# Kernel tuning notes

Hardware: AMD Instinct MI355X
Metric: run time of the kernel (lower is better)

Reference implementation:

```python
import jax, jax.numpy as jnp
import numpy as np

N = 100000
D = 512
B = 64
L = 2048

def setup_inputs() -> dict:
    key = jax.random.key(0)
    k1, k2, k3 = jax.random.split(key, 3)
    gcn_hidden = jax.random.normal(k1, (N, D), dtype=jnp.float32)
    token_position = jax.random.randint(k2, (2 * N,), 0, B, dtype=jnp.int64)
    token_position2 = jax.random.randint(k3, (2 * N,), 0, B, dtype=jnp.int64)
    return {
        "gcn_hidden": gcn_hidden,
        "token_position": token_position,
        "batch_size": B,
        "max_length": L,
        "token_position2": token_position2,
    }

def reference(gcn_hidden, token_position, batch_size, max_length, token_position2):
    # repeat each node row twice consecutively: [N, D] -> [2N, D]
    g2 = jnp.repeat(gcn_hidden, 2, axis=0)
    # scatter-sum rows into batch_size segments: [2N, D] -> [B, D]
    x = jax.ops.segment_sum(g2, token_position, num_segments=batch_size)
    # broadcast across sequence length: [B, D] -> [B, L, D]
    return jnp.broadcast_to(x[:, None, :], (batch_size, max_length, g2.shape[1]))
```

## Files before the change

### kernel.cpp

```cpp
#include <hip/hip_runtime.h>

#define D_DIM    512
#define B_DIM    64
#define L_DIM    2048
#define NBLK1    256
#define THREADS1 512
#define MAXCHUNK 512
#define XSZ      (B_DIM * D_DIM)

typedef float f32x4 __attribute__((ext_vector_type(4)));

__device__ __forceinline__ void rmw2(float* acc, int ia, int ib, float v) {
    float ra = acc[ia];
    float rb = acc[ib];
    float addb = (ia == ib) ? (v + v) : v;
    acc[ia] = ra + v;
    acc[ib] = rb + addb;
}

__global__ __launch_bounds__(THREADS1)
void seg_sum_kernel(const float* __restrict__ g, const int* __restrict__ tp,
                    float* __restrict__ dst, int N, int chunk, int use_atomic) {
    __shared__ float acc[XSZ];
    __shared__ int   pos[2 * MAXCHUNK];
    const int tid = threadIdx.x;

    for (int i = tid; i < XSZ; i += THREADS1) acc[i] = 0.0f;

    int start = blockIdx.x * chunk;
    int end   = start + chunk; if (end > N) end = N;
    int n     = end - start;
    for (int i = tid; i < 2 * n; i += THREADS1) pos[i] = tp[2 * start + i];
    __syncthreads();

    const float* gp = g + (size_t)start * D_DIM + tid;

    int i = 0;
    for (; i + 8 <= n; i += 8) {
        float v0 = gp[(size_t)(i + 0) * D_DIM];
        float v1 = gp[(size_t)(i + 1) * D_DIM];
        float v2 = gp[(size_t)(i + 2) * D_DIM];
        float v3 = gp[(size_t)(i + 3) * D_DIM];
        float v4 = gp[(size_t)(i + 4) * D_DIM];
        float v5 = gp[(size_t)(i + 5) * D_DIM];
        float v6 = gp[(size_t)(i + 6) * D_DIM];
        float v7 = gp[(size_t)(i + 7) * D_DIM];
        rmw2(acc, pos[2*i+ 0] * D_DIM + tid, pos[2*i+ 1] * D_DIM + tid, v0);
        rmw2(acc, pos[2*i+ 2] * D_DIM + tid, pos[2*i+ 3] * D_DIM + tid, v1);
        rmw2(acc, pos[2*i+ 4] * D_DIM + tid, pos[2*i+ 5] * D_DIM + tid, v2);
        rmw2(acc, pos[2*i+ 6] * D_DIM + tid, pos[2*i+ 7] * D_DIM + tid, v3);
        rmw2(acc, pos[2*i+ 8] * D_DIM + tid, pos[2*i+ 9] * D_DIM + tid, v4);
        rmw2(acc, pos[2*i+10] * D_DIM + tid, pos[2*i+11] * D_DIM + tid, v5);
        rmw2(acc, pos[2*i+12] * D_DIM + tid, pos[2*i+13] * D_DIM + tid, v6);
        rmw2(acc, pos[2*i+14] * D_DIM + tid, pos[2*i+15] * D_DIM + tid, v7);
    }
    for (; i < n; ++i) {
        float v = gp[(size_t)i * D_DIM];
        rmw2(acc, pos[2*i + 0] * D_DIM + tid, pos[2*i + 1] * D_DIM + tid, v);
    }
    __syncthreads();

    if (use_atomic) {
        for (int j = tid; j < XSZ; j += THREADS1) {
            float v = acc[j];
            if (v != 0.0f) atomicAdd(&dst[j], v);
        }
    } else {
        f32x4* outp = (f32x4*)(dst + (size_t)blockIdx.x * XSZ);
        const f32x4* a4 = (const f32x4*)acc;
        for (int j = tid; j < XSZ / 4; j += THREADS1) outp[j] = a4[j];
    }
}

__global__ __launch_bounds__(128)
void reduce_partials(const float* __restrict__ p, float* __restrict__ x) {
    int j = blockIdx.x * 128 + threadIdx.x;
    const float* pj = p + j;
    float s = 0.0f;
    #pragma unroll 8
    for (int k = 0; k < NBLK1; ++k) s += pj[(size_t)k * XSZ];
    x[j] = s;
}

#define BC_BLOCKS  1024
#define BC_THREADS 256
__global__ __launch_bounds__(BC_THREADS)
void bcast_lin(const float* __restrict__ x, f32x4* __restrict__ out) {
    int gw   = (blockIdx.x * BC_THREADS + threadIdx.x) >> 6;
    int lane = threadIdx.x & 63;
    size_t base = (size_t)gw * 4096;
    int b = (int)(base >> 18);

    const f32x4* x4 = (const f32x4*)x;
    f32x4 v0 = x4[(b << 7) | lane];
    f32x4 v1 = x4[(b << 7) | (64 + lane)];

    f32x4* o = out + base + lane;
    #pragma unroll 8
    for (int t = 0; t < 64; t += 2) {
        __builtin_nontemporal_store(v0, &o[(size_t)t * 64]);
        __builtin_nontemporal_store(v1, &o[(size_t)t * 64 + 64]);
    }
}

extern "C" void kernel_launch(void* const* d_in, const int* in_sizes, int n_in,
                              void* d_out, int out_size, void* d_ws, size_t ws_size,
                              hipStream_t stream) {
    const float* g   = (const float*)d_in[0];
    const int*   tp  = (const int*)d_in[1];
    float*       out = (float*)d_out;

    int N = in_sizes[1] / 2;
    int chunk = (N + NBLK1 - 1) / NBLK1;

    const size_t need = (size_t)(NBLK1 + 1) * XSZ * sizeof(float);

    if (ws_size >= need) {
        float* partials = (float*)d_ws;
        float* x        = partials + (size_t)NBLK1 * XSZ;
        seg_sum_kernel<<<NBLK1, THREADS1, 0, stream>>>(g, tp, partials, N, chunk, 0);
        reduce_partials<<<XSZ / 128, 128, 0, stream>>>(partials, x);
        bcast_lin<<<BC_BLOCKS, BC_THREADS, 0, stream>>>(x, (f32x4*)out);
    } else {
        float* x = (float*)d_ws;
        (void)hipMemsetAsync(d_ws, 0, XSZ * sizeof(float), stream);
        seg_sum_kernel<<<NBLK1, THREADS1, 0, stream>>>(g, tp, x, N, chunk, 1);
        bcast_lin<<<BC_BLOCKS, BC_THREADS, 0, stream>>>(x, (f32x4*)out);
    }
}
```

Baseline: 434.7 us.

## Split partial reduction across K groups and fold final sum into broadcast

The partial-sum reduction is split into KSPLIT=8 slices, giving 8x more blocks of 256 threads, each summing 32 partials instead of 256. The final 8-way sum moves into the broadcast kernel, which now loops over the parts before writing. Position pairs are loaded as int2 vectors from shared memory, and the broadcast stores change from nontemporal to ordinary stores. The aim is more parallelism in the short reduction kernel. The cost is extra reads in the broadcast kernel and possibly different cache behaviour on the large 33 MB output write.

```diff
diff --git a/kernel.cpp b/kernel.cpp
--- a/kernel.cpp
+++ b/kernel.cpp
@@ -7,6 +7,7 @@
 #define THREADS1 512
 #define MAXCHUNK 512
 #define XSZ      (B_DIM * D_DIM)
+#define KSPLIT   8
 
 typedef float f32x4 __attribute__((ext_vector_type(4)));
 
@@ -22,7 +23,7 @@
 void seg_sum_kernel(const float* __restrict__ g, const int* __restrict__ tp,
                     float* __restrict__ dst, int N, int chunk, int use_atomic) {
     __shared__ float acc[XSZ];
-    __shared__ int   pos[2 * MAXCHUNK];
+    __shared__ int2  pos2[MAXCHUNK];
     const int tid = threadIdx.x;
 
     for (int i = tid; i < XSZ; i += THREADS1) acc[i] = 0.0f;
@@ -30,7 +31,8 @@
     int start = blockIdx.x * chunk;
     int end   = start + chunk; if (end > N) end = N;
     int n     = end - start;
-    for (int i = tid; i < 2 * n; i += THREADS1) pos[i] = tp[2 * start + i];
+    const int2* tp2 = (const int2*)(tp + 2 * start);
+    for (int i = tid; i < n; i += THREADS1) pos2[i] = tp2[i];
     __syncthreads();
 
     const float* gp = g + (size_t)start * D_DIM + tid;
@@ -45,18 +47,21 @@
         float v5 = gp[(size_t)(i + 5) * D_DIM];
         float v6 = gp[(size_t)(i + 6) * D_DIM];
         float v7 = gp[(size_t)(i + 7) * D_DIM];
-        rmw2(acc, pos[2*i+ 0] * D_DIM + tid, pos[2*i+ 1] * D_DIM + tid, v0);
-        rmw2(acc, pos[2*i+ 2] * D_DIM + tid, pos[2*i+ 3] * D_DIM + tid, v1);
-        rmw2(acc, pos[2*i+ 4] * D_DIM + tid, pos[2*i+ 5] * D_DIM + tid, v2);
-        rmw2(acc, pos[2*i+ 6] * D_DIM + tid, pos[2*i+ 7] * D_DIM + tid, v3);
-        rmw2(acc, pos[2*i+ 8] * D_DIM + tid, pos[2*i+ 9] * D_DIM + tid, v4);
-        rmw2(acc, pos[2*i+10] * D_DIM + tid, pos[2*i+11] * D_DIM + tid, v5);
-        rmw2(acc, pos[2*i+12] * D_DIM + tid, pos[2*i+13] * D_DIM + tid, v6);
-        rmw2(acc, pos[2*i+14] * D_DIM + tid, pos[2*i+15] * D_DIM + tid, v7);
+        int2 p0 = pos2[i+0], p1 = pos2[i+1], p2 = pos2[i+2], p3 = pos2[i+3];
+        int2 p4 = pos2[i+4], p5 = pos2[i+5], p6 = pos2[i+6], p7 = pos2[i+7];
+        rmw2(acc, p0.x * D_DIM + tid, p0.y * D_DIM + tid, v0);
+        rmw2(acc, p1.x * D_DIM + tid, p1.y * D_DIM + tid, v1);
+        rmw2(acc, p2.x * D_DIM + tid, p2.y * D_DIM + tid, v2);
+        rmw2(acc, p3.x * D_DIM + tid, p3.y * D_DIM + tid, v3);
+        rmw2(acc, p4.x * D_DIM + tid, p4.y * D_DIM + tid, v4);
+        rmw2(acc, p5.x * D_DIM + tid, p5.y * D_DIM + tid, v5);
+        rmw2(acc, p6.x * D_DIM + tid, p6.y * D_DIM + tid, v6);
+        rmw2(acc, p7.x * D_DIM + tid, p7.y * D_DIM + tid, v7);
     }
     for (; i < n; ++i) {
         float v = gp[(size_t)i * D_DIM];
-        rmw2(acc, pos[2*i + 0] * D_DIM + tid, pos[2*i + 1] * D_DIM + tid, v);
+        int2 p = pos2[i];
+        rmw2(acc, p.x * D_DIM + tid, p.y * D_DIM + tid, v);
     }
     __syncthreads();
 
@@ -72,34 +77,40 @@
     }
 }
 
-__global__ __launch_bounds__(128)
-void reduce_partials(const float* __restrict__ p, float* __restrict__ x) {
-    int j = blockIdx.x * 128 + threadIdx.x;
-    const float* pj = p + j;
+__global__ __launch_bounds__(256)
+void reduce_partials(const float* __restrict__ p, float* __restrict__ xp) {
+    const int jblks = XSZ / 256;
+    int jblk = blockIdx.x & (jblks - 1);
+    int ks   = blockIdx.x >> 7;
+    int j    = (jblk << 8) + threadIdx.x;
+    const float* pj = p + j + (size_t)ks * (NBLK1 / KSPLIT) * XSZ;
     float s = 0.0f;
     #pragma unroll 8
-    for (int k = 0; k < NBLK1; ++k) s += pj[(size_t)k * XSZ];
-    x[j] = s;
+    for (int k = 0; k < NBLK1 / KSPLIT; ++k) s += pj[(size_t)k * XSZ];
+    xp[(size_t)ks * XSZ + j] = s;
 }
 
 #define BC_BLOCKS  1024
 #define BC_THREADS 256
 __global__ __launch_bounds__(BC_THREADS)
-void bcast_lin(const float* __restrict__ x, f32x4* __restrict__ out) {
+void bcast_lin(const float* __restrict__ xp, int nparts, f32x4* __restrict__ out) {
     int gw   = (blockIdx.x * BC_THREADS + threadIdx.x) >> 6;
     int lane = threadIdx.x & 63;
     size_t base = (size_t)gw * 4096;
     int b = (int)(base >> 18);
 
-    const f32x4* x4 = (const f32x4*)x;
-    f32x4 v0 = x4[(b << 7) | lane];
-    f32x4 v1 = x4[(b << 7) | (64 + lane)];
+    const f32x4* x4 = (const f32x4*)xp;
+    f32x4 v0 = 0.0f, v1 = 0.0f;
+    for (int p = 0; p < nparts; ++p) {
+        v0 += x4[(size_t)p * (XSZ / 4) + (b << 7) + lane];
+        v1 += x4[(size_t)p * (XSZ / 4) + (b << 7) + 64 + lane];
+    }
 
     f32x4* o = out + base + lane;
     #pragma unroll 8
     for (int t = 0; t < 64; t += 2) {
-        __builtin_nontemporal_store(v0, &o[(size_t)t * 64]);
-        __builtin_nontemporal_store(v1, &o[(size_t)t * 64 + 64]);
+        o[(size_t)t * 64]      = v0;
+        o[(size_t)t * 64 + 64] = v1;
     }
 }
 
@@ -113,18 +124,18 @@
     int N = in_sizes[1] / 2;
     int chunk = (N + NBLK1 - 1) / NBLK1;
 
-    const size_t need = (size_t)(NBLK1 + 1) * XSZ * sizeof(float);
+    const size_t need = (size_t)(NBLK1 + KSPLIT) * XSZ * sizeof(float);
 
     if (ws_size >= need) {
         float* partials = (float*)d_ws;
-        float* x        = partials + (size_t)NBLK1 * XSZ;
+        float* xp       = partials + (size_t)NBLK1 * XSZ;
         seg_sum_kernel<<<NBLK1, THREADS1, 0, stream>>>(g, tp, partials, N, chunk, 0);
-        reduce_partials<<<XSZ / 128, 128, 0, stream>>>(partials, x);
-        bcast_lin<<<BC_BLOCKS, BC_THREADS, 0, stream>>>(x, (f32x4*)out);
+        reduce_partials<<<(XSZ / 256) * KSPLIT, 256, 0, stream>>>(partials, xp);
+        bcast_lin<<<BC_BLOCKS, BC_THREADS, 0, stream>>>(xp, KSPLIT, (f32x4*)out);
     } else {
         float* x = (float*)d_ws;
         (void)hipMemsetAsync(d_ws, 0, XSZ * sizeof(float), stream);
         seg_sum_kernel<<<NBLK1, THREADS1, 0, stream>>>(g, tp, x, N, chunk, 1);
-        bcast_lin<<<BC_BLOCKS, BC_THREADS, 0, stream>>>(x, (f32x4*)out);
+        bcast_lin<<<BC_BLOCKS, BC_THREADS, 0, stream>>>(x, 1, (f32x4*)out);
     }
 }
```

Result: no change. 438.2 us (+0.8%).
